# Kernel tuning notes

Measured on AMD Instinct MI355X. Metric: run time of the kernel, lower is better.

Reference implementation:

```python
import jax, jax.numpy as jnp
import numpy as np

D_MODEL = 768
NUM_HEADS = 12
D_K = D_MODEL // NUM_HEADS


def setup_inputs() -> dict:
    key = jax.random.key(0)
    ks = jax.random.split(key, 11)
    B, S = 2, 2048
    sc = 1.0 / np.sqrt(D_MODEL)
    return {
        "q": jax.random.normal(ks[0], (B, S, D_MODEL), jnp.float32),
        "k": jax.random.normal(ks[1], (B, S, D_MODEL), jnp.float32),
        "v": jax.random.normal(ks[2], (B, S, D_MODEL), jnp.float32),
        "w_q": jax.random.normal(ks[3], (D_MODEL, D_MODEL), jnp.float32) * sc,
        "b_q": jnp.zeros((D_MODEL,), jnp.float32),
        "w_k": jax.random.normal(ks[4], (D_MODEL, D_MODEL), jnp.float32) * sc,
        "b_k": jnp.zeros((D_MODEL,), jnp.float32),
        "w_v": jax.random.normal(ks[5], (D_MODEL, D_MODEL), jnp.float32) * sc,
        "b_v": jnp.zeros((D_MODEL,), jnp.float32),
        "w_o": jax.random.normal(ks[6], (D_MODEL, D_MODEL), jnp.float32) * sc,
        "b_o": jnp.zeros((D_MODEL,), jnp.float32),
    }


def _split_heads(x, B):
    # [B, S, D] -> [B, H, S, d_k]
    return x.reshape(B, -1, NUM_HEADS, D_K).transpose(0, 2, 1, 3)


def reference(q, k, v, w_q, b_q, w_k, b_k, w_v, b_v, w_o, b_o):
    B = q.shape[0]
    # torch nn.Linear: y = x @ W.T + b; weights stored [out, in]
    qh = _split_heads(q @ w_q.T + b_q, B)
    kh = _split_heads(k @ w_k.T + b_k, B)
    vh = _split_heads(v @ w_v.T + b_v, B)
    scores = jnp.einsum("bhsd,bhtd->bhst", qh, kh) / jnp.sqrt(jnp.float32(D_K))
    attn = jax.nn.softmax(scores, axis=-1)
    ctx = jnp.einsum("bhst,bhtd->bhsd", attn, vh)
    ctx = ctx.transpose(0, 2, 1, 3).reshape(B, -1, D_MODEL)
    return ctx @ w_o.T + b_o
```

## Files before the change

kernel.cpp:

```cpp
#include <hip/hip_runtime.h>
#include <cstdint>


#define S_LEN 2048
#define NHEAD 12
#define DMODEL 768

typedef short s16x8 __attribute__((ext_vector_type(8)));
typedef float f32x4 __attribute__((ext_vector_type(4)));

#define MFMA16(a, b, c) __builtin_amdgcn_mfma_f32_16x16x32_bf16((a), (b), (c), 0, 0, 0)

__device__ __forceinline__ unsigned int pk_bf16(float a, float b) {
  unsigned int ua = __float_as_uint(a), ub = __float_as_uint(b);
  ua = (ua + 0x7FFFu + ((ua >> 16) & 1u)) >> 16;
  ub = (ub + 0x7FFFu + ((ub >> 16) & 1u)) >> 16;
  return ua | (ub << 16);
}
__device__ __forceinline__ short bf16r(float a) {
  unsigned int ua = __float_as_uint(a);
  return (short)((ua + 0x7FFFu + ((ua >> 16) & 1u)) >> 16);
}
__device__ __forceinline__ unsigned int pk_trunc(float a, float b) {
  return __builtin_amdgcn_perm(__float_as_uint(b), __float_as_uint(a), 0x07060302u);
}
__device__ __forceinline__ float bf16_floor(float a) {
  return __uint_as_float(__float_as_uint(a) & 0xFFFF0000u);
}

__global__ __launch_bounds__(256)
void convert_w(const float* __restrict__ w0, const float* __restrict__ w1,
               const float* __restrict__ w2, const float* __restrict__ w3,
               short* __restrict__ o0, short* __restrict__ o1,
               short* __restrict__ o2, short* __restrict__ o3) {
  const float* src = (blockIdx.y == 0) ? w0 : (blockIdx.y == 1) ? w1
                   : (blockIdx.y == 2) ? w2 : w3;
  short* dst = (blockIdx.y == 0) ? o0 : (blockIdx.y == 1) ? o1
             : (blockIdx.y == 2) ? o2 : o3;
  const long i = ((long)blockIdx.x * 256 + threadIdx.x) * 4;
  float4 f = *(const float4*)(src + i);
  uint2 u;
  u.x = pk_bf16(f.x, f.y);
  u.y = pk_bf16(f.z, f.w);
  *(uint2*)(dst + i) = u;
}

template <bool ABF>
__device__ __forceinline__ void gemm64x128(const void* __restrict__ Av,
                                           const short* __restrict__ Bv,
                                           int m0, int n0, f32x4 (&acc)[2][4],
                                           short* Alds, short* Blds) {
  constexpr int K = 768;
  const int tid  = threadIdx.x;
  const int lane = tid & 63;
  const int w    = tid >> 6;
  const int g    = lane >> 4;
  const int c    = lane & 15;
  const int wm   = (w & 1) * 32;
  const int wn   = (w >> 1) * 64;

#pragma unroll
  for (int i = 0; i < 2; ++i)
#pragma unroll
    for (int j = 0; j < 4; ++j) acc[i][j] = (f32x4){0.f, 0.f, 0.f, 0.f};

  const int arow = tid >> 2, acol = (tid & 3) * 8;
  const int brow = tid >> 1, bcol = (tid & 1) * 16;

  for (int kt = 0; kt < K; kt += 32) {
    if (ABF) {
      const short* Ap = (const short*)Av + (long)(m0 + arow) * K + kt + acol;
      *(uint4*)&Alds[arow * 40 + acol] = *(const uint4*)Ap;
    } else {
      const float* Ap = (const float*)Av + (long)(m0 + arow) * K + kt + acol;
      float4 f0 = ((const float4*)Ap)[0];
      float4 f1 = ((const float4*)Ap)[1];
      uint4 u;
      u.x = pk_bf16(f0.x, f0.y); u.y = pk_bf16(f0.z, f0.w);
      u.z = pk_bf16(f1.x, f1.y); u.w = pk_bf16(f1.z, f1.w);
      *(uint4*)&Alds[arow * 40 + acol] = u;
    }
    {
      const short* Bp = Bv + (long)(n0 + brow) * K + kt + bcol;
      *(uint4*)&Blds[brow * 40 + bcol]     = *(const uint4*)Bp;
      *(uint4*)&Blds[brow * 40 + bcol + 8] = *(const uint4*)(Bp + 8);
    }
    __syncthreads();

    s16x8 af[2], bf[4];
#pragma unroll
    for (int mb = 0; mb < 2; ++mb)
      af[mb] = *(const s16x8*)&Alds[(wm + mb * 16 + c) * 40 + g * 8];
#pragma unroll
    for (int nb = 0; nb < 4; ++nb)
      bf[nb] = *(const s16x8*)&Blds[(wn + nb * 16 + c) * 40 + g * 8];
#pragma unroll
    for (int mb = 0; mb < 2; ++mb)
#pragma unroll
      for (int nb = 0; nb < 4; ++nb)
        acc[mb][nb] = MFMA16(af[mb], bf[nb], acc[mb][nb]);
    __syncthreads();
  }
}

__global__ __launch_bounds__(256)
void qkv_kernel(const float* __restrict__ q, const float* __restrict__ k,
                const float* __restrict__ v,
                const short* __restrict__ wq, const short* __restrict__ wk,
                const short* __restrict__ wv,
                const float* __restrict__ bq, const float* __restrict__ bk,
                const float* __restrict__ bv,
                short* __restrict__ qh, short* __restrict__ kh,
                short* __restrict__ vt) {
  __shared__ short Alds[64 * 40];
  __shared__ short Blds[128 * 40];
  const int z = blockIdx.z;
  const float* A = (z == 0) ? q : (z == 1) ? k : v;
  const short* B = (z == 0) ? wq : (z == 1) ? wk : wv;
  const float* bias = (z == 0) ? bq : (z == 1) ? bk : bv;

  const int m0 = blockIdx.y * 64;
  const int n0 = blockIdx.x * 128;
  f32x4 acc[2][4];
  gemm64x128<false>(A, B, m0, n0, acc, Alds, Blds);

  const int lane = threadIdx.x & 63, w = threadIdx.x >> 6;
  const int g = lane >> 4, c = lane & 15;
  const int wm = (w & 1) * 32, wn = (w >> 1) * 64;

  if (z < 2) {
    short* outp = z ? kh : qh;
    const float scale = z ? 1.0f : 0.18033688011112042f;
#pragma unroll
    for (int mb = 0; mb < 2; ++mb) {
#pragma unroll
      for (int nb = 0; nb < 4; ++nb) {
        const int n = n0 + wn + nb * 16 + c;
        const float bvv = bias[n];
        const int hh = n >> 6, d = n & 63;
#pragma unroll
        for (int r = 0; r < 4; ++r) {
          const int m = m0 + wm + mb * 16 + g * 4 + r;
          const int b = m >> 11, s = m & 2047;
          const float val = (acc[mb][nb][r] + bvv) * scale;
          outp[(((long)(b * NHEAD + hh) * S_LEN + s) << 6) + d] = bf16r(val);
        }
      }
    }
  } else {
#pragma unroll
    for (int mb = 0; mb < 2; ++mb) {
#pragma unroll
      for (int nb = 0; nb < 4; ++nb) {
        const int n = n0 + wn + nb * 16 + c;
        const float bvv = bias[n];
        const int hh = n >> 6, d = n & 63;
        const int m_base = m0 + wm + mb * 16 + g * 4;
        const int b = m_base >> 11, t = m_base & 2047;
        uint2 ov;
        ov.x = pk_bf16(acc[mb][nb][0] + bvv, acc[mb][nb][1] + bvv);
        ov.y = pk_bf16(acc[mb][nb][2] + bvv, acc[mb][nb][3] + bvv);
        *(uint2*)(vt + ((long)(b * NHEAD + hh) * 64 + d) * S_LEN + t) = ov;
      }
    }
  }
}

__global__ __launch_bounds__(256)
void o_kernel(const short* __restrict__ ctx, const short* __restrict__ wo,
              const float* __restrict__ bo, float* __restrict__ out) {
  __shared__ short Alds[64 * 40];
  __shared__ short Blds[128 * 40];
  const int m0 = blockIdx.y * 64;
  const int n0 = blockIdx.x * 128;
  f32x4 acc[2][4];
  gemm64x128<true>(ctx, wo, m0, n0, acc, Alds, Blds);

  const int lane = threadIdx.x & 63, w = threadIdx.x >> 6;
  const int g = lane >> 4, c = lane & 15;
  const int wm = (w & 1) * 32, wn = (w >> 1) * 64;
#pragma unroll
  for (int mb = 0; mb < 2; ++mb) {
#pragma unroll
    for (int nb = 0; nb < 4; ++nb) {
      const int n = n0 + wn + nb * 16 + c;
      const float bvv = bo[n];
#pragma unroll
      for (int r = 0; r < 4; ++r) {
        const int m = m0 + wm + mb * 16 + g * 4 + r;
        out[(long)m * DMODEL + n] = acc[mb][nb][r] + bvv;
      }
    }
  }
}

__global__ __launch_bounds__(256)
void attn_kernel(const short* __restrict__ Qh, const short* __restrict__ Kh,
                 const short* __restrict__ Vt, short* __restrict__ Ctx) {
  __shared__ short kbuf[2][64 * 64];
  __shared__ short vbuf[2][64 * 64];
  __shared__ short pbuf[4][16 * 72];

  const int tid  = threadIdx.x;
  const int lane = tid & 63;
  const int w    = tid >> 6;
  const int g    = lane >> 4;
  const int c    = lane & 15;
  const int bh   = blockIdx.y;
  const int qs0  = blockIdx.x * 64;
  const long base = (long)bh * S_LEN * 64;
  const short* Qb = Qh + base;
  const short* Kb = Kh + base;
  const short* Vb = Vt + base;

  const long qrow = (long)(qs0 + w * 16 + c) * 64;
  const s16x8 qf0 = *(const s16x8*)(Qb + qrow + g * 8);
  const s16x8 qf1 = *(const s16x8*)(Qb + qrow + 32 + g * 8);

  f32x4 co[4];
#pragma unroll
  for (int i = 0; i < 4; ++i) co[i] = (f32x4){0.f, 0.f, 0.f, 0.f};
  float l_lane = 0.f;

  const int srow = tid >> 2;
  const int sq   = tid & 3;
  const int sw   = srow & 7;
  const int sg0  = ((2 * sq)     ^ sw) * 8;
  const int sg1  = ((2 * sq + 1) ^ sw) * 8;
  const int cw   = c & 7;
  const int rg0  = ((g)     ^ cw) * 8;
  const int rg1  = ((4 + g) ^ cw) * 8;

  const short* kg = Kb + (long)srow * 64 + sq * 16;
  const short* vg = Vb + (long)srow * S_LEN + sq * 16;

  {
    uint4 ka = *(const uint4*)kg;
    uint4 kb2 = *(const uint4*)(kg + 8);
    uint4 va = *(const uint4*)vg;
    uint4 vb2 = *(const uint4*)(vg + 8);
    *(uint4*)&kbuf[0][srow * 64 + sg0] = ka;
    *(uint4*)&kbuf[0][srow * 64 + sg1] = kb2;
    *(uint4*)&vbuf[0][srow * 64 + sg0] = va;
    *(uint4*)&vbuf[0][srow * 64 + sg1] = vb2;
  }

  for (int it = 0; it < S_LEN / 64; ++it) {
    const int cur = it & 1;
    const long tn = (it + 1 < S_LEN / 64) ? (long)(it + 1) * 64 : 0;
    uint4 nka = *(const uint4*)(kg + tn * 64);
    uint4 nkb = *(const uint4*)(kg + tn * 64 + 8);
    uint4 nva = *(const uint4*)(vg + tn);
    uint4 nvb = *(const uint4*)(vg + tn + 8);
    __syncthreads();

    f32x4 st[4];
#pragma unroll
    for (int mb = 0; mb < 4; ++mb) {
      const s16x8 k0 = *(const s16x8*)&kbuf[cur][(mb * 16 + c) * 64 + rg0];
      const s16x8 k1 = *(const s16x8*)&kbuf[cur][(mb * 16 + c) * 64 + rg1];
      f32x4 z = (f32x4){0.f, 0.f, 0.f, 0.f};
      z = MFMA16(k0, qf0, z);
      z = MFMA16(k1, qf1, z);
      st[mb] = z;
    }

#pragma unroll
    for (int mb = 0; mb < 4; ++mb) {
      float p0 = __builtin_amdgcn_exp2f(st[mb][0]);
      float p1 = __builtin_amdgcn_exp2f(st[mb][1]);
      float p2 = __builtin_amdgcn_exp2f(st[mb][2]);
      float p3 = __builtin_amdgcn_exp2f(st[mb][3]);
      l_lane += bf16_floor(p0) + bf16_floor(p1) + bf16_floor(p2) + bf16_floor(p3);
      uint2 pw;
      pw.x = pk_trunc(p0, p1);
      pw.y = pk_trunc(p2, p3);
      *(uint2*)&pbuf[w][c * 72 + mb * 16 + g * 4] = pw;
    }
    const s16x8 pb0 = *(const s16x8*)&pbuf[w][c * 72 + g * 8];
    const s16x8 pb1 = *(const s16x8*)&pbuf[w][c * 72 + 32 + g * 8];

#pragma unroll
    for (int db = 0; db < 4; ++db) {
      const s16x8 v0 = *(const s16x8*)&vbuf[cur][(db * 16 + c) * 64 + rg0];
      const s16x8 v1 = *(const s16x8*)&vbuf[cur][(db * 16 + c) * 64 + rg1];
      co[db] = MFMA16(v0, pb0, co[db]);
      co[db] = MFMA16(v1, pb1, co[db]);
    }

    *(uint4*)&kbuf[cur ^ 1][srow * 64 + sg0] = nka;
    *(uint4*)&kbuf[cur ^ 1][srow * 64 + sg1] = nkb;
    *(uint4*)&vbuf[cur ^ 1][srow * 64 + sg0] = nva;
    *(uint4*)&vbuf[cur ^ 1][srow * 64 + sg1] = nvb;
  }

  float rs = l_lane;
  rs += __shfl_xor(rs, 16);
  rs += __shfl_xor(rs, 32);
  const float invl = 1.f / rs;

  const int hh = bh % NHEAD;
  const long tok = (long)(bh / NHEAD) * S_LEN + qs0 + w * 16 + c;
#pragma unroll
  for (int db = 0; db < 4; ++db) {
    uint2 ov;
    ov.x = pk_bf16(co[db][0] * invl, co[db][1] * invl);
    ov.y = pk_bf16(co[db][2] * invl, co[db][3] * invl);
    *(uint2*)(Ctx + tok * DMODEL + hh * 64 + db * 16 + g * 4) = ov;
  }
}

extern "C" void kernel_launch(void* const* d_in, const int* in_sizes, int n_in,
                              void* d_out, int out_size, void* d_ws, size_t ws_size,
                              hipStream_t stream) {
  const float* q   = (const float*)d_in[0];
  const float* k   = (const float*)d_in[1];
  const float* v   = (const float*)d_in[2];
  const float* w_q = (const float*)d_in[3];
  const float* b_q = (const float*)d_in[4];
  const float* w_k = (const float*)d_in[5];
  const float* b_k = (const float*)d_in[6];
  const float* w_v = (const float*)d_in[7];
  const float* b_v = (const float*)d_in[8];
  const float* w_o = (const float*)d_in[9];
  const float* b_o = (const float*)d_in[10];
  float* out = (float*)d_out;

  const long NELEM = (long)2 * NHEAD * S_LEN * 64;
  const long WELEM = (long)DMODEL * DMODEL;
  short* qh  = (short*)d_ws;
  short* kh  = qh + NELEM;
  short* vt  = kh + NELEM;
  short* ctx = vt + NELEM;
  short* wqb = ctx + NELEM;
  short* wkb = wqb + WELEM;
  short* wvb = wkb + WELEM;
  short* wob = wvb + WELEM;

  dim3 blk(256);
  convert_w<<<dim3(576, 4), blk, 0, stream>>>(w_q, w_k, w_v, w_o,
                                              wqb, wkb, wvb, wob);
  qkv_kernel<<<dim3(6, 64, 3), blk, 0, stream>>>(q, k, v, wqb, wkb, wvb,
                                                 b_q, b_k, b_v, qh, kh, vt);
  attn_kernel<<<dim3(32, 24), blk, 0, stream>>>(qh, kh, vt, ctx);
  o_kernel<<<dim3(6, 64), blk, 0, stream>>>(ctx, wob, b_o, out);
}
```

Baseline: 218.8 us.

## Use 128x128 double-buffered GEMM tiles with XCD-aware block remapping

Replaces the 64x128 single-buffered projection GEMM with a 128x128 tile that prefetches the next K-slice into registers and alternates between two LDS buffers, so only one barrier per iteration remains. Launches flattened 1-D grids whose block index is remapped so that consecutive tiles sharing A rows land on the same XCD, which should improve L2 reuse. The larger tile raises register and LDS use and halves the block count, which may lower occupancy and tail balance.

```diff
diff --git a/kernel.cpp b/kernel.cpp
--- a/kernel.cpp
+++ b/kernel.cpp
@@ -46,60 +46,90 @@
 }
 
 template <bool ABF>
-__device__ __forceinline__ void gemm64x128(const void* __restrict__ Av,
-                                           const short* __restrict__ Bv,
-                                           int m0, int n0, f32x4 (&acc)[2][4],
-                                           short* Alds, short* Blds) {
+__device__ __forceinline__ void gemm128db(const void* __restrict__ Av,
+                                          const short* __restrict__ Bv,
+                                          int m0, int n0, f32x4 (&acc)[4][4],
+                                          short* Alds, short* Blds) {
   constexpr int K = 768;
+  constexpr int NIT = K / 32;
   const int tid  = threadIdx.x;
   const int lane = tid & 63;
   const int w    = tid >> 6;
   const int g    = lane >> 4;
   const int c    = lane & 15;
-  const int wm   = (w & 1) * 32;
+  const int wm   = (w & 1) * 64;
   const int wn   = (w >> 1) * 64;
-
-#pragma unroll
-  for (int i = 0; i < 2; ++i)
+  const int srow = tid >> 1;
+  const int sc   = (tid & 1) * 16;
+
+#pragma unroll
+  for (int i = 0; i < 4; ++i)
 #pragma unroll
     for (int j = 0; j < 4; ++j) acc[i][j] = (f32x4){0.f, 0.f, 0.f, 0.f};
 
-  const int arow = tid >> 2, acol = (tid & 3) * 8;
-  const int brow = tid >> 1, bcol = (tid & 1) * 16;
-
-  for (int kt = 0; kt < K; kt += 32) {
+  float4 rf[4];
+  uint4 ra0, ra1;
+  uint4 rb0, rb1;
+
+  auto fetch = [&](int kt) {
     if (ABF) {
-      const short* Ap = (const short*)Av + (long)(m0 + arow) * K + kt + acol;
-      *(uint4*)&Alds[arow * 40 + acol] = *(const uint4*)Ap;
+      const short* Ap = (const short*)Av + (long)(m0 + srow) * K + kt + sc;
+      ra0 = *(const uint4*)Ap;
+      ra1 = *(const uint4*)(Ap + 8);
     } else {
-      const float* Ap = (const float*)Av + (long)(m0 + arow) * K + kt + acol;
-      float4 f0 = ((const float4*)Ap)[0];
-      float4 f1 = ((const float4*)Ap)[1];
-      uint4 u;
-      u.x = pk_bf16(f0.x, f0.y); u.y = pk_bf16(f0.z, f0.w);
-      u.z = pk_bf16(f1.x, f1.y); u.w = pk_bf16(f1.z, f1.w);
-      *(uint4*)&Alds[arow * 40 + acol] = u;
-    }
-    {
-      const short* Bp = Bv + (long)(n0 + brow) * K + kt + bcol;
-      *(uint4*)&Blds[brow * 40 + bcol]     = *(const uint4*)Bp;
-      *(uint4*)&Blds[brow * 40 + bcol + 8] = *(const uint4*)(Bp + 8);
-    }
+      const float* Ap = (const float*)Av + (long)(m0 + srow) * K + kt + sc;
+      rf[0] = ((const float4*)Ap)[0];
+      rf[1] = ((const float4*)Ap)[1];
+      rf[2] = ((const float4*)Ap)[2];
+      rf[3] = ((const float4*)Ap)[3];
+    }
+    const short* Bp = Bv + (long)(n0 + srow) * K + kt + sc;
+    rb0 = *(const uint4*)Bp;
+    rb1 = *(const uint4*)(Bp + 8);
+  };
+  auto store = [&](int buf) {
+    short* Ab = Alds + buf * (128 * 40);
+    short* Bb = Blds + buf * (128 * 40);
+    if (ABF) {
+      *(uint4*)&Ab[srow * 40 + sc]     = ra0;
+      *(uint4*)&Ab[srow * 40 + sc + 8] = ra1;
+    } else {
+      uint4 u0, u1;
+      u0.x = pk_bf16(rf[0].x, rf[0].y); u0.y = pk_bf16(rf[0].z, rf[0].w);
+      u0.z = pk_bf16(rf[1].x, rf[1].y); u0.w = pk_bf16(rf[1].z, rf[1].w);
+      u1.x = pk_bf16(rf[2].x, rf[2].y); u1.y = pk_bf16(rf[2].z, rf[2].w);
+      u1.z = pk_bf16(rf[3].x, rf[3].y); u1.w = pk_bf16(rf[3].z, rf[3].w);
+      *(uint4*)&Ab[srow * 40 + sc]     = u0;
+      *(uint4*)&Ab[srow * 40 + sc + 8] = u1;
+    }
+    *(uint4*)&Bb[srow * 40 + sc]     = rb0;
+    *(uint4*)&Bb[srow * 40 + sc + 8] = rb1;
+  };
+
+  fetch(0);
+  store(0);
+  for (int it = 0; it < NIT; ++it) {
+    const int cur = it & 1;
+    const int ktn = (it + 1 < NIT) ? (it + 1) * 32 : 0;
+    fetch(ktn);
     __syncthreads();
 
-    s16x8 af[2], bf[4];
-#pragma unroll
-    for (int mb = 0; mb < 2; ++mb)
-      af[mb] = *(const s16x8*)&Alds[(wm + mb * 16 + c) * 40 + g * 8];
+    const short* Ab = Alds + cur * (128 * 40);
+    const short* Bb = Blds + cur * (128 * 40);
+    s16x8 af[4], bf[4];
+#pragma unroll
+    for (int mb = 0; mb < 4; ++mb)
+      af[mb] = *(const s16x8*)&Ab[(wm + mb * 16 + c) * 40 + g * 8];
 #pragma unroll
     for (int nb = 0; nb < 4; ++nb)
-      bf[nb] = *(const s16x8*)&Blds[(wn + nb * 16 + c) * 40 + g * 8];
-#pragma unroll
-    for (int mb = 0; mb < 2; ++mb)
+      bf[nb] = *(const s16x8*)&Bb[(wn + nb * 16 + c) * 40 + g * 8];
+#pragma unroll
+    for (int mb = 0; mb < 4; ++mb)
 #pragma unroll
       for (int nb = 0; nb < 4; ++nb)
         acc[mb][nb] = MFMA16(af[mb], bf[nb], acc[mb][nb]);
-    __syncthreads();
+
+    store(cur ^ 1);
   }
 }
 
@@ -112,27 +142,35 @@
                 const float* __restrict__ bv,
                 short* __restrict__ qh, short* __restrict__ kh,
                 short* __restrict__ vt) {
-  __shared__ short Alds[64 * 40];
-  __shared__ short Blds[128 * 40];
-  const int z = blockIdx.z;
+  __shared__ short Alds[2 * 128 * 40];
+  __shared__ short Blds[2 * 128 * 40];
+
+  const int L   = blockIdx.x;
+  const int xcd = L & 7;
+  const int i   = L >> 3;
+  const int nt  = i % 6;
+  const int gp  = xcd * 12 + i / 6;
+  const int z   = gp / 32;
+  const int mt  = gp % 32;
+  const int m0  = mt * 128;
+  const int n0  = nt * 128;
+
   const float* A = (z == 0) ? q : (z == 1) ? k : v;
   const short* B = (z == 0) ? wq : (z == 1) ? wk : wv;
   const float* bias = (z == 0) ? bq : (z == 1) ? bk : bv;
 
-  const int m0 = blockIdx.y * 64;
-  const int n0 = blockIdx.x * 128;
-  f32x4 acc[2][4];
-  gemm64x128<false>(A, B, m0, n0, acc, Alds, Blds);
+  f32x4 acc[4][4];
+  gemm128db<false>(A, B, m0, n0, acc, Alds, Blds);
 
   const int lane = threadIdx.x & 63, w = threadIdx.x >> 6;
   const int g = lane >> 4, c = lane & 15;
-  const int wm = (w & 1) * 32, wn = (w >> 1) * 64;
+  const int wm = (w & 1) * 64, wn = (w >> 1) * 64;
 
   if (z < 2) {
     short* outp = z ? kh : qh;
     const float scale = z ? 1.0f : 0.18033688011112042f;
 #pragma unroll
-    for (int mb = 0; mb < 2; ++mb) {
+    for (int mb = 0; mb < 4; ++mb) {
 #pragma unroll
       for (int nb = 0; nb < 4; ++nb) {
         const int n = n0 + wn + nb * 16 + c;
@@ -149,7 +187,7 @@
     }
   } else {
 #pragma unroll
-    for (int mb = 0; mb < 2; ++mb) {
+    for (int mb = 0; mb < 4; ++mb) {
 #pragma unroll
       for (int nb = 0; nb < 4; ++nb) {
         const int n = n0 + wn + nb * 16 + c;
@@ -169,18 +207,25 @@
 __global__ __launch_bounds__(256)
 void o_kernel(const short* __restrict__ ctx, const short* __restrict__ wo,
               const float* __restrict__ bo, float* __restrict__ out) {
-  __shared__ short Alds[64 * 40];
-  __shared__ short Blds[128 * 40];
-  const int m0 = blockIdx.y * 64;
-  const int n0 = blockIdx.x * 128;
-  f32x4 acc[2][4];
-  gemm64x128<true>(ctx, wo, m0, n0, acc, Alds, Blds);
+  __shared__ short Alds[2 * 128 * 40];
+  __shared__ short Blds[2 * 128 * 40];
+
+  const int L   = blockIdx.x;
+  const int xcd = L & 7;
+  const int i   = L >> 3;
+  const int nt  = i % 6;
+  const int mt  = xcd * 4 + i / 6;
+  const int m0  = mt * 128;
+  const int n0  = nt * 128;
+
+  f32x4 acc[4][4];
+  gemm128db<true>(ctx, wo, m0, n0, acc, Alds, Blds);
 
   const int lane = threadIdx.x & 63, w = threadIdx.x >> 6;
   const int g = lane >> 4, c = lane & 15;
-  const int wm = (w & 1) * 32, wn = (w >> 1) * 64;
-#pragma unroll
-  for (int mb = 0; mb < 2; ++mb) {
+  const int wm = (w & 1) * 64, wn = (w >> 1) * 64;
+#pragma unroll
+  for (int mb = 0; mb < 4; ++mb) {
 #pragma unroll
     for (int nb = 0; nb < 4; ++nb) {
       const int n = n0 + wn + nb * 16 + c;
@@ -340,8 +385,8 @@
   dim3 blk(256);
   convert_w<<<dim3(576, 4), blk, 0, stream>>>(w_q, w_k, w_v, w_o,
                                               wqb, wkb, wvb, wob);
-  qkv_kernel<<<dim3(6, 64, 3), blk, 0, stream>>>(q, k, v, wqb, wkb, wvb,
-                                                 b_q, b_k, b_v, qh, kh, vt);
+  qkv_kernel<<<dim3(576), blk, 0, stream>>>(q, k, v, wqb, wkb, wvb,
+                                            b_q, b_k, b_v, qh, kh, vt);
   attn_kernel<<<dim3(32, 24), blk, 0, stream>>>(qh, kh, vt, ctx);
-  o_kernel<<<dim3(6, 64), blk, 0, stream>>>(ctx, wob, b_o, out);
-}
+  o_kernel<<<dim3(192), blk, 0, stream>>>(ctx, wob, b_o, out);
+}
```

New measurement: 211.0 us. -3.6%, faster.

## Double-buffer GEMM LDS with two-deep register prefetch, remap blocks per XCD, swizzle P buffer

Applied to the files above, without the earlier changes.

The projection GEMMs now use double-buffered LDS with a register prefetch two k-steps ahead, which drops one barrier per iteration. The attention K/V loads also prefetch two tiles ahead. Blocks in the QKV and output GEMMs are renumbered so that tiles sharing an A row panel run on the same XCD, which should improve L2 reuse. The attention P staging buffer changes from padded rows to an XOR swizzle, reducing LDS use and bank conflicts. In exchange, more registers and LDS are used per block, which may lower occupancy.

```diff
diff --git a/kernel.cpp b/kernel.cpp
--- a/kernel.cpp
+++ b/kernel.cpp
@@ -46,11 +46,12 @@
 }
 
 template <bool ABF>
-__device__ __forceinline__ void gemm64x128(const void* __restrict__ Av,
-                                           const short* __restrict__ Bv,
-                                           int m0, int n0, f32x4 (&acc)[2][4],
-                                           short* Alds, short* Blds) {
+__device__ __forceinline__ void gemm64x128db(const void* __restrict__ Av,
+                                             const short* __restrict__ Bv,
+                                             int m0, int n0, f32x4 (&acc)[2][4],
+                                             short* Alds, short* Blds) {
   constexpr int K = 768;
+  constexpr int NIT = K / 32;
   const int tid  = threadIdx.x;
   const int lane = tid & 63;
   const int w    = tid >> 6;
@@ -58,48 +59,72 @@
   const int c    = lane & 15;
   const int wm   = (w & 1) * 32;
   const int wn   = (w >> 1) * 64;
+  const int ar   = tid >> 2, ac = (tid & 3) * 8;
+  const int br   = tid >> 1, bc = (tid & 1) * 16;
 
 #pragma unroll
   for (int i = 0; i < 2; ++i)
 #pragma unroll
     for (int j = 0; j < 4; ++j) acc[i][j] = (f32x4){0.f, 0.f, 0.f, 0.f};
 
-  const int arow = tid >> 2, acol = (tid & 3) * 8;
-  const int brow = tid >> 1, bcol = (tid & 1) * 16;
-
-  for (int kt = 0; kt < K; kt += 32) {
+  float4 raf[2][2];
+  uint4  rab[2];
+  uint4  rb[2][2];
+
+  auto fetch = [&](int set, int kt) {
     if (ABF) {
-      const short* Ap = (const short*)Av + (long)(m0 + arow) * K + kt + acol;
-      *(uint4*)&Alds[arow * 40 + acol] = *(const uint4*)Ap;
+      rab[set] = *(const uint4*)((const short*)Av + (long)(m0 + ar) * K + kt + ac);
     } else {
-      const float* Ap = (const float*)Av + (long)(m0 + arow) * K + kt + acol;
-      float4 f0 = ((const float4*)Ap)[0];
-      float4 f1 = ((const float4*)Ap)[1];
+      const float* Ap = (const float*)Av + (long)(m0 + ar) * K + kt + ac;
+      raf[set][0] = ((const float4*)Ap)[0];
+      raf[set][1] = ((const float4*)Ap)[1];
+    }
+    const short* Bp = Bv + (long)(n0 + br) * K + kt + bc;
+    rb[set][0] = *(const uint4*)Bp;
+    rb[set][1] = *(const uint4*)(Bp + 8);
+  };
+  auto store = [&](int set, int buf) {
+    short* Ab = Alds + buf * (64 * 40);
+    short* Bb = Blds + buf * (128 * 40);
+    if (ABF) {
+      *(uint4*)&Ab[ar * 40 + ac] = rab[set];
+    } else {
       uint4 u;
-      u.x = pk_bf16(f0.x, f0.y); u.y = pk_bf16(f0.z, f0.w);
-      u.z = pk_bf16(f1.x, f1.y); u.w = pk_bf16(f1.z, f1.w);
-      *(uint4*)&Alds[arow * 40 + acol] = u;
-    }
-    {
-      const short* Bp = Bv + (long)(n0 + brow) * K + kt + bcol;
-      *(uint4*)&Blds[brow * 40 + bcol]     = *(const uint4*)Bp;
-      *(uint4*)&Blds[brow * 40 + bcol + 8] = *(const uint4*)(Bp + 8);
-    }
+      u.x = pk_bf16(raf[set][0].x, raf[set][0].y);
+      u.y = pk_bf16(raf[set][0].z, raf[set][0].w);
+      u.z = pk_bf16(raf[set][1].x, raf[set][1].y);
+      u.w = pk_bf16(raf[set][1].z, raf[set][1].w);
+      *(uint4*)&Ab[ar * 40 + ac] = u;
+    }
+    *(uint4*)&Bb[br * 40 + bc]     = rb[set][0];
+    *(uint4*)&Bb[br * 40 + bc + 8] = rb[set][1];
+  };
+
+  fetch(0, 0);
+  fetch(1, 32);
+  store(0, 0);
+  for (int it = 0; it < NIT; ++it) {
+    const int cur = it & 1;
     __syncthreads();
-
+    const int kt2 = (it + 2 < NIT) ? (it + 2) * 32 : 0;
+    fetch(cur, kt2);
+
+    const short* Ab = Alds + cur * (64 * 40);
+    const short* Bb = Blds + cur * (128 * 40);
     s16x8 af[2], bf[4];
 #pragma unroll
     for (int mb = 0; mb < 2; ++mb)
-      af[mb] = *(const s16x8*)&Alds[(wm + mb * 16 + c) * 40 + g * 8];
+      af[mb] = *(const s16x8*)&Ab[(wm + mb * 16 + c) * 40 + g * 8];
 #pragma unroll
     for (int nb = 0; nb < 4; ++nb)
-      bf[nb] = *(const s16x8*)&Blds[(wn + nb * 16 + c) * 40 + g * 8];
+      bf[nb] = *(const s16x8*)&Bb[(wn + nb * 16 + c) * 40 + g * 8];
 #pragma unroll
     for (int mb = 0; mb < 2; ++mb)
 #pragma unroll
       for (int nb = 0; nb < 4; ++nb)
         acc[mb][nb] = MFMA16(af[mb], bf[nb], acc[mb][nb]);
-    __syncthreads();
+
+    store(cur ^ 1, cur ^ 1);
   }
 }
 
@@ -112,17 +137,25 @@
                 const float* __restrict__ bv,
                 short* __restrict__ qh, short* __restrict__ kh,
                 short* __restrict__ vt) {
-  __shared__ short Alds[64 * 40];
-  __shared__ short Blds[128 * 40];
-  const int z = blockIdx.z;
+  __shared__ short Alds[2 * 64 * 40];
+  __shared__ short Blds[2 * 128 * 40];
+
+  const int L   = blockIdx.x;
+  const int xcd = L & 7;
+  const int i   = L >> 3;
+  const int nt  = i % 6;
+  const int pl  = xcd * 24 + i / 6;
+  const int z   = pl >> 6;
+  const int mt  = pl & 63;
+  const int m0  = mt * 64;
+  const int n0  = nt * 128;
+
   const float* A = (z == 0) ? q : (z == 1) ? k : v;
   const short* B = (z == 0) ? wq : (z == 1) ? wk : wv;
   const float* bias = (z == 0) ? bq : (z == 1) ? bk : bv;
 
-  const int m0 = blockIdx.y * 64;
-  const int n0 = blockIdx.x * 128;
   f32x4 acc[2][4];
-  gemm64x128<false>(A, B, m0, n0, acc, Alds, Blds);
+  gemm64x128db<false>(A, B, m0, n0, acc, Alds, Blds);
 
   const int lane = threadIdx.x & 63, w = threadIdx.x >> 6;
   const int g = lane >> 4, c = lane & 15;
@@ -169,12 +202,19 @@
 __global__ __launch_bounds__(256)
 void o_kernel(const short* __restrict__ ctx, const short* __restrict__ wo,
               const float* __restrict__ bo, float* __restrict__ out) {
-  __shared__ short Alds[64 * 40];
-  __shared__ short Blds[128 * 40];
-  const int m0 = blockIdx.y * 64;
-  const int n0 = blockIdx.x * 128;
+  __shared__ short Alds[2 * 64 * 40];
+  __shared__ short Blds[2 * 128 * 40];
+
+  const int L   = blockIdx.x;
+  const int xcd = L & 7;
+  const int i   = L >> 3;
+  const int nt  = i % 6;
+  const int mt  = xcd * 8 + i / 6;
+  const int m0  = mt * 64;
+  const int n0  = nt * 128;
+
   f32x4 acc[2][4];
-  gemm64x128<true>(ctx, wo, m0, n0, acc, Alds, Blds);
+  gemm64x128db<true>(ctx, wo, m0, n0, acc, Alds, Blds);
 
   const int lane = threadIdx.x & 63, w = threadIdx.x >> 6;
   const int g = lane >> 4, c = lane & 15;
@@ -199,7 +239,7 @@
                  const short* __restrict__ Vt, short* __restrict__ Ctx) {
   __shared__ short kbuf[2][64 * 64];
   __shared__ short vbuf[2][64 * 64];
-  __shared__ short pbuf[4][16 * 72];
+  __shared__ short pbuf[4][16 * 64];
 
   const int tid  = threadIdx.x;
   const int lane = tid & 63;
@@ -234,25 +274,32 @@
   const short* kg = Kb + (long)srow * 64 + sq * 16;
   const short* vg = Vb + (long)srow * S_LEN + sq * 16;
 
-  {
-    uint4 ka = *(const uint4*)kg;
-    uint4 kb2 = *(const uint4*)(kg + 8);
-    uint4 va = *(const uint4*)vg;
-    uint4 vb2 = *(const uint4*)(vg + 8);
-    *(uint4*)&kbuf[0][srow * 64 + sg0] = ka;
-    *(uint4*)&kbuf[0][srow * 64 + sg1] = kb2;
-    *(uint4*)&vbuf[0][srow * 64 + sg0] = va;
-    *(uint4*)&vbuf[0][srow * 64 + sg1] = vb2;
-  }
+  uint4 rk[2][2], rv[2][2];
+  auto fetchKV = [&](int set, long t0) {
+    rk[set][0] = *(const uint4*)(kg + t0 * 64);
+    rk[set][1] = *(const uint4*)(kg + t0 * 64 + 8);
+    rv[set][0] = *(const uint4*)(vg + t0);
+    rv[set][1] = *(const uint4*)(vg + t0 + 8);
+  };
+  auto storeKV = [&](int set, int buf) {
+    *(uint4*)&kbuf[buf][srow * 64 + sg0] = rk[set][0];
+    *(uint4*)&kbuf[buf][srow * 64 + sg1] = rk[set][1];
+    *(uint4*)&vbuf[buf][srow * 64 + sg0] = rv[set][0];
+    *(uint4*)&vbuf[buf][srow * 64 + sg1] = rv[set][1];
+  };
+
+  fetchKV(0, 0);
+  fetchKV(1, 64);
+  storeKV(0, 0);
+
+  const int pr0 = c * 64 + ((g ^ cw) * 8);
+  const int pr1 = c * 64 + (((4 + g) ^ cw) * 8);
 
   for (int it = 0; it < S_LEN / 64; ++it) {
     const int cur = it & 1;
-    const long tn = (it + 1 < S_LEN / 64) ? (long)(it + 1) * 64 : 0;
-    uint4 nka = *(const uint4*)(kg + tn * 64);
-    uint4 nkb = *(const uint4*)(kg + tn * 64 + 8);
-    uint4 nva = *(const uint4*)(vg + tn);
-    uint4 nvb = *(const uint4*)(vg + tn + 8);
     __syncthreads();
+    const long tn = (it + 2 < S_LEN / 64) ? (long)(it + 2) * 64 : 0;
+    fetchKV(cur, tn);
 
     f32x4 st[4];
 #pragma unroll
@@ -275,10 +322,11 @@
       uint2 pw;
       pw.x = pk_trunc(p0, p1);
       pw.y = pk_trunc(p2, p3);
-      *(uint2*)&pbuf[w][c * 72 + mb * 16 + g * 4] = pw;
-    }
-    const s16x8 pb0 = *(const s16x8*)&pbuf[w][c * 72 + g * 8];
-    const s16x8 pb1 = *(const s16x8*)&pbuf[w][c * 72 + 32 + g * 8];
+      const int pg = ((2 * mb + (g >> 1)) ^ cw) * 8 + (g & 1) * 4;
+      *(uint2*)&pbuf[w][c * 64 + pg] = pw;
+    }
+    const s16x8 pb0 = *(const s16x8*)&pbuf[w][pr0];
+    const s16x8 pb1 = *(const s16x8*)&pbuf[w][pr1];
 
 #pragma unroll
     for (int db = 0; db < 4; ++db) {
@@ -288,10 +336,7 @@
       co[db] = MFMA16(v1, pb1, co[db]);
     }
 
-    *(uint4*)&kbuf[cur ^ 1][srow * 64 + sg0] = nka;
-    *(uint4*)&kbuf[cur ^ 1][srow * 64 + sg1] = nkb;
-    *(uint4*)&vbuf[cur ^ 1][srow * 64 + sg0] = nva;
-    *(uint4*)&vbuf[cur ^ 1][srow * 64 + sg1] = nvb;
+    storeKV(cur ^ 1, cur ^ 1);
   }
 
   float rs = l_lane;
@@ -340,8 +385,8 @@
   dim3 blk(256);
   convert_w<<<dim3(576, 4), blk, 0, stream>>>(w_q, w_k, w_v, w_o,
                                               wqb, wkb, wvb, wob);
-  qkv_kernel<<<dim3(6, 64, 3), blk, 0, stream>>>(q, k, v, wqb, wkb, wvb,
-                                                 b_q, b_k, b_v, qh, kh, vt);
+  qkv_kernel<<<dim3(1152), blk, 0, stream>>>(q, k, v, wqb, wkb, wvb,
+                                             b_q, b_k, b_v, qh, kh, vt);
   attn_kernel<<<dim3(32, 24), blk, 0, stream>>>(qh, kh, vt, ctx);
-  o_kernel<<<dim3(6, 64), blk, 0, stream>>>(ctx, wob, b_o, out);
-}
+  o_kernel<<<dim3(384), blk, 0, stream>>>(ctx, wob, b_o, out);
+}
```

Result: slower. 493.6 us (+125.6%).
